# Kernel optimization log

Hardware: AMD Instinct MI355X
Metric: run time of the kernel (lower is better)

Reference implementation:

```python
import jax, jax.numpy as jnp
import numpy as np

NEG = -1e9  # matches torch masked_fill value (additive, not -inf)

def setup_inputs() -> dict:
    key = jax.random.key(0)
    k1, k2, k3, k4 = jax.random.split(key, 4)
    B, H, S, D = 8, 16, 1024, 64
    q = jax.random.normal(k1, (B, H, S, D), dtype=jnp.float32)
    k = jax.random.normal(k2, (B, H, S, D), dtype=jnp.float32)
    v = jax.random.normal(k3, (B, H, S, D), dtype=jnp.float32)
    event_length = jax.random.randint(k4, (B,), 0, S, dtype=jnp.int32)
    return {"q": q, "k": k, "v": v, "event_length": event_length}

def reference(q, k, v, event_length):
    B, H, S, D = q.shape
    scale = 1.0 / jnp.sqrt(jnp.asarray(D, dtype=q.dtype))
    idx = jnp.arange(S)
    # valid[b, i] = i < event_length[b]
    valid = idx[None, :] < event_length[:, None]            # [B, S]
    # additive mask: 0 where (row valid AND col valid), else -1e9
    pair = valid[:, :, None] & valid[:, None, :]            # [B, S, S]
    attn_mask = jnp.where(pair, 0.0, NEG).astype(q.dtype)[:, None, :, :]  # [B,1,S,S]
    scores = jnp.einsum('bhqd,bhkd->bhqk', q, k) * scale + attn_mask
    probs = jax.nn.softmax(scores, axis=-1)
    out = jnp.einsum('bhqk,bhkd->bhqd', probs, v)
    return out
```

## Files before the change

kernel.cpp:

```cpp
#include <hip/hip_runtime.h>


#define Sdim 1024
#define Ddim 64
#define PITCH 72

typedef float f32x4 __attribute__((ext_vector_type(4)));
typedef _Float16 f16x8 __attribute__((ext_vector_type(8)));
typedef unsigned short u16x8 __attribute__((ext_vector_type(8)));
typedef unsigned int u32x2 __attribute__((ext_vector_type(2)));

union FragU { u16x8 u; f16x8 h; };

__device__ __forceinline__ unsigned pk2(float a, float b) {
  auto h = __builtin_amdgcn_cvt_pkrtz(a, b);
  return __builtin_bit_cast(unsigned, h);
}

__global__ __launch_bounds__(256, 3)
void attn_fwd(const float* __restrict__ Q, const float* __restrict__ K,
              const float* __restrict__ V, const int* __restrict__ EL,
              float* __restrict__ Out) {
  __shared__ unsigned short k_lds[64 * PITCH];
  __shared__ unsigned short v_lds[64 * PITCH];
  __shared__ unsigned short p_lds[4][32 * PITCH];

  const int bid0 = blockIdx.x;
  const int x  = bid0 & 7;
  const int j  = bid0 >> 3;
  const int bh = (j >> 3) * 8 + x;
  const int qt = j & 7;
  const int L  = EL[bh >> 4];

  const int tid  = threadIdx.x;
  const size_t base = (size_t)bh * Sdim * Ddim;
  const float* Qb = Q + base;
  const float* Kb = K + base;
  const float* Vb = V + base;

  const int q0blk = qt * 128;

  if (q0blk >= L) {
    float* red = (float*)k_lds;
    const int sc4 = (tid & 15) * 4;
    const int rg0 = tid >> 4;
    const float* vp = Vb + (size_t)rg0 * Ddim + sc4;
    float4 acc = {0.f, 0.f, 0.f, 0.f};
#pragma unroll 8
    for (int i = 0; i < 64; ++i) {
      float4 a = *(const float4*)(vp + (size_t)i * 16 * Ddim);
      acc.x += a.x; acc.y += a.y; acc.z += a.z; acc.w += a.w;
    }
    *(float4*)&red[rg0 * 68 + sc4] = acc;
    __syncthreads();
    if (tid < 16) {
      float4 s = {0.f, 0.f, 0.f, 0.f};
#pragma unroll
      for (int i = 0; i < 16; ++i) {
        float4 a = *(const float4*)&red[i * 68 + tid * 4];
        s.x += a.x; s.y += a.y; s.z += a.z; s.w += a.w;
      }
      const float inv = 1.0f / 1024.0f;
      s.x *= inv; s.y *= inv; s.z *= inv; s.w *= inv;
      *(float4*)&red[16 * 68 + tid * 4] = s;
    }
    __syncthreads();
    const float4 cm = *(const float4*)&red[16 * 68 + sc4];
    float* ob = Out + base;
#pragma unroll
    for (int p = 0; p < 8; ++p) {
      int row = q0blk + p * 16 + rg0;
      *(float4*)&ob[(size_t)row * Ddim + sc4] = cm;
    }
    return;
  }

  const int w    = tid >> 6;
  const int lane = tid & 63;
  const int r    = lane & 15;
  const int hi   = lane >> 4;

  const int q0w      = q0blk + w * 32;
  const bool wValid  = q0w < L;
  const bool wAllVal = (q0w + 32) <= L;
  const int kFull    = (L + 63) >> 6;
  const int kFullW   = wValid ? kFull : 0;
  const int ntiles   = (q0blk + 128 <= L) ? kFull : 16;
  const int ktB      = L >> 6;

  const bool qv0 = (q0w + r) < L;
  const bool qv1 = (q0w + 16 + r) < L;

  const float SCL = 0.125f * 1.44269504088896340736f;
  f16x8 qf[2][2];
  if (wValid) {
#pragma unroll
    for (int qc = 0; qc < 2; ++qc)
#pragma unroll
      for (int kk = 0; kk < 2; ++kk) {
        const float* p = Qb + (size_t)(q0w + qc * 16 + r) * Ddim + kk * 32 + hi * 8;
        float4 a = *(const float4*)p;
        float4 c = *(const float4*)(p + 4);
        union { unsigned u[4]; f16x8 h; } f;
        f.u[0] = pk2(a.x * SCL, a.y * SCL); f.u[1] = pk2(a.z * SCL, a.w * SCL);
        f.u[2] = pk2(c.x * SCL, c.y * SCL); f.u[3] = pk2(c.z * SCL, c.w * SCL);
        qf[qc][kk] = f.h;
      }
  }

  const f32x4 zero4 = {0.f, 0.f, 0.f, 0.f};
  f32x4 oacc[2][4];
#pragma unroll
  for (int qc = 0; qc < 2; ++qc)
#pragma unroll
    for (int dc = 0; dc < 4; ++dc) oacc[qc][dc] = zero4;

  float lpart[2] = {0.f, 0.f};

  const int sr = tid >> 4, sc = tid & 15;
  const float* pK = Kb + (size_t)sr * Ddim + sc * 4;
  const float* pV = Vb + (size_t)(sr * 4) * Ddim + sc * 4;

  float4 kpre[4], vpre[4];
  auto LOADK = [&](int k0_) {
#pragma unroll
    for (int i = 0; i < 4; ++i)
      kpre[i] = *(const float4*)(pK + (size_t)(k0_ + 16 * i) * Ddim);
  };
  auto LOADV = [&](int k0_) {
#pragma unroll
    for (int jj = 0; jj < 4; ++jj)
      vpre[jj] = *(const float4*)(pV + (size_t)(k0_ + jj) * Ddim);
  };

  LOADK(0);
  LOADV(0);

  for (int kt = 0; kt < ntiles; ++kt) {
    const int k0 = kt * 64;
    const bool fullB = kt < kFull;
    const bool fullW = kt < kFullW;
    __syncthreads();

    if (fullB) {
#pragma unroll
      for (int i = 0; i < 4; ++i) {
        u32x2 o;
        o[0] = pk2(kpre[i].x, kpre[i].y); o[1] = pk2(kpre[i].z, kpre[i].w);
        *(u32x2*)&k_lds[(16 * i + sr) * PITCH + sc * 4] = o;
      }
    }
    {
      u32x2 o;
      o[0] = pk2(vpre[0].x, vpre[1].x); o[1] = pk2(vpre[2].x, vpre[3].x);
      *(u32x2*)&v_lds[(sc * 4 + 0) * PITCH + sr * 4] = o;
      o[0] = pk2(vpre[0].y, vpre[1].y); o[1] = pk2(vpre[2].y, vpre[3].y);
      *(u32x2*)&v_lds[(sc * 4 + 1) * PITCH + sr * 4] = o;
      o[0] = pk2(vpre[0].z, vpre[1].z); o[1] = pk2(vpre[2].z, vpre[3].z);
      *(u32x2*)&v_lds[(sc * 4 + 2) * PITCH + sr * 4] = o;
      o[0] = pk2(vpre[0].w, vpre[1].w); o[1] = pk2(vpre[2].w, vpre[3].w);
      *(u32x2*)&v_lds[(sc * 4 + 3) * PITCH + sr * 4] = o;
    }
    __syncthreads();

    if (kt + 1 < kFull)  LOADK(k0 + 64);
    if (kt + 1 < ntiles) LOADV(k0 + 64);

    if (fullW) {
      f32x4 sacc[2][4];
#pragma unroll
      for (int qc = 0; qc < 2; ++qc)
#pragma unroll
        for (int kc = 0; kc < 4; ++kc) sacc[qc][kc] = zero4;

      __builtin_amdgcn_s_setprio(1);
#pragma unroll
      for (int kc = 0; kc < 4; ++kc)
#pragma unroll
        for (int kk = 0; kk < 2; ++kk) {
          FragU kf;
          kf.u = *(const u16x8*)&k_lds[(kc * 16 + r) * PITCH + kk * 32 + hi * 8];
          sacc[0][kc] = __builtin_amdgcn_mfma_f32_16x16x32_f16(kf.h, qf[0][kk], sacc[0][kc], 0, 0, 0);
          sacc[1][kc] = __builtin_amdgcn_mfma_f32_16x16x32_f16(kf.h, qf[1][kk], sacc[1][kc], 0, 0, 0);
        }
      __builtin_amdgcn_s_setprio(0);

      const bool noMask = wAllVal && (kt != ktB);
#pragma unroll
      for (int qc = 0; qc < 2; ++qc) {
        const bool qv = qc ? qv1 : qv0;
        float ls = 0.f;
#pragma unroll
        for (int kc = 0; kc < 4; ++kc) {
          float p[4];
#pragma unroll
          for (int rg = 0; rg < 4; ++rg) {
            float s = sacc[qc][kc][rg];
            if (!noMask) {
              int kg = k0 + kc * 16 + 4 * hi + rg;
              s = qv ? ((kg < L) ? s : -__builtin_inff()) : 0.0f;
            }
            p[rg] = exp2f(s);
            ls += p[rg];
          }
          u32x2 o;
          o[0] = pk2(p[0], p[1]);
          o[1] = pk2(p[2], p[3]);
          *(u32x2*)&p_lds[w][(qc * 16 + r) * PITCH + kc * 16 + 4 * hi] = o;
        }
        lpart[qc] += ls;
      }
    } else {
      if (kt == kFullW) {
        unsigned p0 = pk2(qv0 ? 0.f : 1.f, qv0 ? 0.f : 1.f);
        unsigned p1 = pk2(qv1 ? 0.f : 1.f, qv1 ? 0.f : 1.f);
#pragma unroll
        for (int kc = 0; kc < 4; ++kc) {
          u32x2 o0; o0[0] = p0; o0[1] = p0;
          u32x2 o1; o1[0] = p1; o1[1] = p1;
          *(u32x2*)&p_lds[w][(r) * PITCH + kc * 16 + 4 * hi] = o0;
          *(u32x2*)&p_lds[w][(16 + r) * PITCH + kc * 16 + 4 * hi] = o1;
        }
      }
      lpart[0] += qv0 ? 0.f : 16.f;
      lpart[1] += qv1 ? 0.f : 16.f;
    }

    asm volatile("s_waitcnt lgkmcnt(0)" ::: "memory");
    __builtin_amdgcn_sched_barrier(0);

    __builtin_amdgcn_s_setprio(1);
#pragma unroll
    for (int ks = 0; ks < 2; ++ks) {
      FragU pf0, pf1;
      pf0.u = *(const u16x8*)&p_lds[w][(0  + r) * PITCH + ks * 32 + hi * 8];
      pf1.u = *(const u16x8*)&p_lds[w][(16 + r) * PITCH + ks * 32 + hi * 8];
#pragma unroll
      for (int dc = 0; dc < 4; ++dc) {
        FragU vf;
        vf.u = *(const u16x8*)&v_lds[(dc * 16 + r) * PITCH + ks * 32 + hi * 8];
        oacc[0][dc] = __builtin_amdgcn_mfma_f32_16x16x32_f16(pf0.h, vf.h, oacc[0][dc], 0, 0, 0);
        oacc[1][dc] = __builtin_amdgcn_mfma_f32_16x16x32_f16(pf1.h, vf.h, oacc[1][dc], 0, 0, 0);
      }
    }
    __builtin_amdgcn_s_setprio(0);
  }

  float* ob = Out + base;
#pragma unroll
  for (int qc = 0; qc < 2; ++qc) {
    float l = lpart[qc];
    l += __shfl_xor(l, 16, 64);
    l += __shfl_xor(l, 32, 64);
#pragma unroll
    for (int rg = 0; rg < 4; ++rg) {
      float lsq = __shfl(l, 4 * hi + rg, 64);
      float inv = 1.0f / lsq;
      int qrow = q0w + qc * 16 + 4 * hi + rg;
#pragma unroll
      for (int dc = 0; dc < 4; ++dc)
        ob[(size_t)qrow * Ddim + dc * 16 + r] = oacc[qc][dc][rg] * inv;
    }
  }
}

extern "C" void kernel_launch(void* const* d_in, const int* in_sizes, int n_in,
                              void* d_out, int out_size, void* d_ws, size_t ws_size,
                              hipStream_t stream) {
  const float* q  = (const float*)d_in[0];
  const float* k  = (const float*)d_in[1];
  const float* v  = (const float*)d_in[2];
  const int*   el = (const int*)d_in[3];
  float* out = (float*)d_out;
  dim3 grid(8 * 16 * (Sdim / 128));
  dim3 block(256);
  hipLaunchKernelGGL(attn_fwd, grid, block, 0, stream, q, k, v, el, out);
}
```

Measured before the change: 55.66 us.

## Handle straddling query blocks with column-mean path and swizzle tile order

In query blocks that straddle the valid length, invalid rows are no longer run through all 16 key tiles. Instead the loop stops at the valid key tiles and the invalid rows are filled from a separate mean-of-V reduction. The query-tile index is also XOR-swizzled by the block-pair index so heavy and light blocks spread more evenly across the dispatch order. The cost is an extra full V read for straddling blocks and slightly more branching.

```diff
diff --git a/kernel.cpp b/kernel.cpp
--- a/kernel.cpp
+++ b/kernel.cpp
@@ -28,8 +28,9 @@
   const int bid0 = blockIdx.x;
   const int x  = bid0 & 7;
   const int j  = bid0 >> 3;
-  const int bh = (j >> 3) * 8 + x;
-  const int qt = j & 7;
+  const int p  = j >> 3;
+  const int qt = (j & 7) ^ ((p >> 1) & 7);
+  const int bh = p * 8 + x;
   const int L  = EL[bh >> 4];
 
   const int tid  = threadIdx.x;
@@ -68,8 +69,8 @@
     const float4 cm = *(const float4*)&red[16 * 68 + sc4];
     float* ob = Out + base;
 #pragma unroll
-    for (int p = 0; p < 8; ++p) {
-      int row = q0blk + p * 16 + rg0;
+    for (int pp = 0; pp < 8; ++pp) {
+      int row = q0blk + pp * 16 + rg0;
       *(float4*)&ob[(size_t)row * Ddim + sc4] = cm;
     }
     return;
@@ -84,12 +85,11 @@
   const bool wValid  = q0w < L;
   const bool wAllVal = (q0w + 32) <= L;
   const int kFull    = (L + 63) >> 6;
-  const int kFullW   = wValid ? kFull : 0;
-  const int ntiles   = (q0blk + 128 <= L) ? kFull : 16;
   const int ktB      = L >> 6;
 
   const bool qv0 = (q0w + r) < L;
   const bool qv1 = (q0w + 16 + r) < L;
+  const bool straddle = (q0blk + 128) > L;
 
   const float SCL = 0.125f * 1.44269504088896340736f;
   f16x8 qf[2][2];
@@ -98,9 +98,9 @@
     for (int qc = 0; qc < 2; ++qc)
 #pragma unroll
       for (int kk = 0; kk < 2; ++kk) {
-        const float* p = Qb + (size_t)(q0w + qc * 16 + r) * Ddim + kk * 32 + hi * 8;
-        float4 a = *(const float4*)p;
-        float4 c = *(const float4*)(p + 4);
+        const float* pq = Qb + (size_t)(q0w + qc * 16 + r) * Ddim + kk * 32 + hi * 8;
+        float4 a = *(const float4*)pq;
+        float4 c = *(const float4*)(pq + 4);
         union { unsigned u[4]; f16x8 h; } f;
         f.u[0] = pk2(a.x * SCL, a.y * SCL); f.u[1] = pk2(a.z * SCL, a.w * SCL);
         f.u[2] = pk2(c.x * SCL, c.y * SCL); f.u[3] = pk2(c.z * SCL, c.w * SCL);
@@ -136,19 +136,15 @@
   LOADK(0);
   LOADV(0);
 
-  for (int kt = 0; kt < ntiles; ++kt) {
+  for (int kt = 0; kt < kFull; ++kt) {
     const int k0 = kt * 64;
-    const bool fullB = kt < kFull;
-    const bool fullW = kt < kFullW;
-    __syncthreads();
-
-    if (fullB) {
-#pragma unroll
-      for (int i = 0; i < 4; ++i) {
-        u32x2 o;
-        o[0] = pk2(kpre[i].x, kpre[i].y); o[1] = pk2(kpre[i].z, kpre[i].w);
-        *(u32x2*)&k_lds[(16 * i + sr) * PITCH + sc * 4] = o;
-      }
+    __syncthreads();
+
+#pragma unroll
+    for (int i = 0; i < 4; ++i) {
+      u32x2 o;
+      o[0] = pk2(kpre[i].x, kpre[i].y); o[1] = pk2(kpre[i].z, kpre[i].w);
+      *(u32x2*)&k_lds[(16 * i + sr) * PITCH + sc * 4] = o;
     }
     {
       u32x2 o;
@@ -163,10 +159,9 @@
     }
     __syncthreads();
 
-    if (kt + 1 < kFull)  LOADK(k0 + 64);
-    if (kt + 1 < ntiles) LOADV(k0 + 64);
-
-    if (fullW) {
+    if (kt + 1 < kFull) { LOADK(k0 + 64); LOADV(k0 + 64); }
+
+    if (wValid) {
       f32x4 sacc[2][4];
 #pragma unroll
       for (int qc = 0; qc < 2; ++qc)
@@ -192,58 +187,44 @@
         float ls = 0.f;
 #pragma unroll
         for (int kc = 0; kc < 4; ++kc) {
-          float p[4];
+          float pr[4];
 #pragma unroll
           for (int rg = 0; rg < 4; ++rg) {
             float s = sacc[qc][kc][rg];
             if (!noMask) {
               int kg = k0 + kc * 16 + 4 * hi + rg;
-              s = qv ? ((kg < L) ? s : -__builtin_inff()) : 0.0f;
+              s = (qv && kg < L) ? s : -__builtin_inff();
             }
-            p[rg] = exp2f(s);
-            ls += p[rg];
+            pr[rg] = exp2f(s);
+            ls += pr[rg];
           }
           u32x2 o;
-          o[0] = pk2(p[0], p[1]);
-          o[1] = pk2(p[2], p[3]);
+          o[0] = pk2(pr[0], pr[1]);
+          o[1] = pk2(pr[2], pr[3]);
           *(u32x2*)&p_lds[w][(qc * 16 + r) * PITCH + kc * 16 + 4 * hi] = o;
         }
         lpart[qc] += ls;
       }
-    } else {
-      if (kt == kFullW) {
-        unsigned p0 = pk2(qv0 ? 0.f : 1.f, qv0 ? 0.f : 1.f);
-        unsigned p1 = pk2(qv1 ? 0.f : 1.f, qv1 ? 0.f : 1.f);
-#pragma unroll
-        for (int kc = 0; kc < 4; ++kc) {
-          u32x2 o0; o0[0] = p0; o0[1] = p0;
-          u32x2 o1; o1[0] = p1; o1[1] = p1;
-          *(u32x2*)&p_lds[w][(r) * PITCH + kc * 16 + 4 * hi] = o0;
-          *(u32x2*)&p_lds[w][(16 + r) * PITCH + kc * 16 + 4 * hi] = o1;
+
+      asm volatile("s_waitcnt lgkmcnt(0)" ::: "memory");
+      __builtin_amdgcn_sched_barrier(0);
+
+      __builtin_amdgcn_s_setprio(1);
+#pragma unroll
+      for (int ks = 0; ks < 2; ++ks) {
+        FragU pf0, pf1;
+        pf0.u = *(const u16x8*)&p_lds[w][(0  + r) * PITCH + ks * 32 + hi * 8];
+        pf1.u = *(const u16x8*)&p_lds[w][(16 + r) * PITCH + ks * 32 + hi * 8];
+#pragma unroll
+        for (int dc = 0; dc < 4; ++dc) {
+          FragU vf;
+          vf.u = *(const u16x8*)&v_lds[(dc * 16 + r) * PITCH + ks * 32 + hi * 8];
+          oacc[0][dc] = __builtin_amdgcn_mfma_f32_16x16x32_f16(pf0.h, vf.h, oacc[0][dc], 0, 0, 0);
+          oacc[1][dc] = __builtin_amdgcn_mfma_f32_16x16x32_f16(pf1.h, vf.h, oacc[1][dc], 0, 0, 0);
         }
       }
-      lpart[0] += qv0 ? 0.f : 16.f;
-      lpart[1] += qv1 ? 0.f : 16.f;
-    }
-
-    asm volatile("s_waitcnt lgkmcnt(0)" ::: "memory");
-    __builtin_amdgcn_sched_barrier(0);
-
-    __builtin_amdgcn_s_setprio(1);
-#pragma unroll
-    for (int ks = 0; ks < 2; ++ks) {
-      FragU pf0, pf1;
-      pf0.u = *(const u16x8*)&p_lds[w][(0  + r) * PITCH + ks * 32 + hi * 8];
-      pf1.u = *(const u16x8*)&p_lds[w][(16 + r) * PITCH + ks * 32 + hi * 8];
-#pragma unroll
-      for (int dc = 0; dc < 4; ++dc) {
-        FragU vf;
-        vf.u = *(const u16x8*)&v_lds[(dc * 16 + r) * PITCH + ks * 32 + hi * 8];
-        oacc[0][dc] = __builtin_amdgcn_mfma_f32_16x16x32_f16(pf0.h, vf.h, oacc[0][dc], 0, 0, 0);
-        oacc[1][dc] = __builtin_amdgcn_mfma_f32_16x16x32_f16(pf1.h, vf.h, oacc[1][dc], 0, 0, 0);
-      }
-    }
-    __builtin_amdgcn_s_setprio(0);
+      __builtin_amdgcn_s_setprio(0);
+    }
   }
 
   float* ob = Out + base;
@@ -257,9 +238,46 @@
       float lsq = __shfl(l, 4 * hi + rg, 64);
       float inv = 1.0f / lsq;
       int qrow = q0w + qc * 16 + 4 * hi + rg;
-#pragma unroll
-      for (int dc = 0; dc < 4; ++dc)
-        ob[(size_t)qrow * Ddim + dc * 16 + r] = oacc[qc][dc][rg] * inv;
+      if (qrow < L) {
+#pragma unroll
+        for (int dc = 0; dc < 4; ++dc)
+          ob[(size_t)qrow * Ddim + dc * 16 + r] = oacc[qc][dc][rg] * inv;
+      }
+    }
+  }
+
+  if (straddle) {
+    __syncthreads();
+    float* red = (float*)k_lds;
+    const int sc4 = (tid & 15) * 4;
+    const int rg0 = tid >> 4;
+    const float* vp = Vb + (size_t)rg0 * Ddim + sc4;
+    float4 acc = {0.f, 0.f, 0.f, 0.f};
+#pragma unroll 8
+    for (int i = 0; i < 64; ++i) {
+      float4 a = *(const float4*)(vp + (size_t)i * 16 * Ddim);
+      acc.x += a.x; acc.y += a.y; acc.z += a.z; acc.w += a.w;
+    }
+    *(float4*)&red[rg0 * 68 + sc4] = acc;
+    __syncthreads();
+    if (tid < 16) {
+      float4 s = {0.f, 0.f, 0.f, 0.f};
+#pragma unroll
+      for (int i = 0; i < 16; ++i) {
+        float4 a = *(const float4*)&red[i * 68 + tid * 4];
+        s.x += a.x; s.y += a.y; s.z += a.z; s.w += a.w;
+      }
+      const float inv = 1.0f / 1024.0f;
+      s.x *= inv; s.y *= inv; s.z *= inv; s.w *= inv;
+      *(float4*)&red[16 * 68 + tid * 4] = s;
+    }
+    __syncthreads();
+    const float4 cm = *(const float4*)&red[16 * 68 + sc4];
+#pragma unroll
+    for (int pp = 0; pp < 8; ++pp) {
+      int row = q0blk + pp * 16 + rg0;
+      if (row >= L)
+        *(float4*)&ob[(size_t)row * Ddim + sc4] = cm;
     }
   }
 }
```

Measured after the change: 51.25 us. 7.9% less time.
